# Kernel tuning notes

Hardware: AMD Instinct MI355X
Metric: run time of the kernel (lower is better)

Reference implementation:

```python
import jax, jax.numpy as jnp
import numpy as np

B, L, N, D, H, DFF, LAYERS, PRED = 16, 96, 512, 512, 8, 2048, 2, 96
NMARK = 4
WINDOWS = (4, 8, 12, 24)
EPS_REVIN = 1e-5


def layernorm(x, g, b, eps=1e-5):
    m = x.mean(-1, keepdims=True)
    v = ((x - m) ** 2).mean(-1, keepdims=True)
    return (x - m) * jax.lax.rsqrt(v + eps) * g + b


def moving_avg(x, w):
    # replicate-pad left by w-1, then window-mean of size w (stride 1) -> same length
    p = jnp.pad(x, ((0, 0), (w - 1, 0), (0, 0)), mode='edge')
    c = jnp.cumsum(p, axis=1)
    c = jnp.concatenate([jnp.zeros_like(c[:, :1]), c], axis=1)
    return (c[:, w:] - c[:, :-w]) / w


def trend_guidance(x, w1, b1, w2, b2):
    # x: [B, L, N]
    trend_stack = jnp.stack([moving_avg(x, w) for w in WINDOWS], axis=-1)  # [B,L,N,W]
    mean_f = x.mean(axis=1)
    std_f = jnp.sqrt(x.var(axis=1) + 1e-6)
    stats = jnp.stack([mean_f, std_f], axis=-1)  # [B,N,2]
    h = jax.nn.relu(stats @ w1 + b1)
    weights = jax.nn.softmax(h @ w2 + b2, axis=-1)  # [B,N,W]
    trend = (trend_stack * weights[:, None]).sum(-1)  # [B,L,N]
    tf = trend.transpose(0, 2, 1)  # [B,N,L]
    nt = tf / jnp.maximum(jnp.linalg.norm(tf, axis=-1, keepdims=True), 1e-12)
    return nt @ nt.transpose(0, 2, 1)  # [B,N,N]


def enc_layer(x, guide_full, wq, bq, wk, bk, wv, bv, wo, bo, w1, b1, w2, b2, l1g, l1b, l2g, l2b):
    Bq, T, Dm = x.shape
    E = Dm // H
    q = (x @ wq + bq).reshape(Bq, T, H, E)
    k = (x @ wk + bk).reshape(Bq, T, H, E)
    v = (x @ wv + bv).reshape(Bq, T, H, E)
    scores = jnp.einsum('blhe,bshe->bhls', q, k) / jnp.sqrt(jnp.asarray(E, x.dtype))
    attn = jax.nn.softmax(scores, axis=-1)
    attn = attn * guide_full[:, None]                      # sigmoid guidance gate
    attn = attn / (attn.sum(-1, keepdims=True) + 1e-6)     # renormalize
    ctx = jnp.einsum('bhls,bshd->blhd', attn, v).reshape(Bq, T, Dm)
    x = x + (ctx @ wo + bo)
    x = layernorm(x, l1g, l1b)
    y = jax.nn.gelu(x @ w1 + b1, approximate=False)
    y = y @ w2 + b2
    return layernorm(x + y, l2g, l2b)


def setup_inputs():
    key = jax.random.key(0)
    ks = iter(jax.random.split(key, 64))
    def nrm(shape, s=0.02):
        return jax.random.normal(next(ks), shape, jnp.float32) * s
    return {
        'x_enc': jax.random.normal(next(ks), (B, L, N), jnp.float32),
        'x_mark_enc': jax.random.normal(next(ks), (B, L, NMARK), jnp.float32),
        'x_dec': jnp.zeros((1, 1, 1), jnp.float32),
        'x_mark_dec': jnp.zeros((1, 1, 1), jnp.float32),
        'gamma': jnp.ones((1, 1, N), jnp.float32),
        'beta': jnp.zeros((1, 1, N), jnp.float32),
        'tp_w1': nrm((2, 16), 0.5), 'tp_b1': jnp.zeros((16,), jnp.float32),
        'tp_w2': nrm((16, len(WINDOWS)), 0.5), 'tp_b2': jnp.zeros((len(WINDOWS),), jnp.float32),
        'emb_w': nrm((L, D)), 'emb_b': jnp.zeros((D,), jnp.float32),
        'wq': nrm((LAYERS, D, D)), 'bq': jnp.zeros((LAYERS, D), jnp.float32),
        'wk': nrm((LAYERS, D, D)), 'bk': jnp.zeros((LAYERS, D), jnp.float32),
        'wv': nrm((LAYERS, D, D)), 'bv': jnp.zeros((LAYERS, D), jnp.float32),
        'wo': nrm((LAYERS, D, D)), 'bo': jnp.zeros((LAYERS, D), jnp.float32),
        'w1': nrm((LAYERS, D, DFF)), 'b1': jnp.zeros((LAYERS, DFF), jnp.float32),
        'w2': nrm((LAYERS, DFF, D)), 'b2': jnp.zeros((LAYERS, D), jnp.float32),
        'ln1g': jnp.ones((LAYERS, D), jnp.float32), 'ln1b': jnp.zeros((LAYERS, D), jnp.float32),
        'ln2g': jnp.ones((LAYERS, D), jnp.float32), 'ln2b': jnp.zeros((LAYERS, D), jnp.float32),
        'normg': jnp.ones((D,), jnp.float32), 'normb': jnp.zeros((D,), jnp.float32),
        'proj_w': nrm((D, PRED)), 'proj_b': jnp.zeros((PRED,), jnp.float32),
    }


def reference(x_enc, x_mark_enc, x_dec, x_mark_dec, gamma, beta, tp_w1, tp_b1, tp_w2, tp_b2,
              emb_w, emb_b, wq, bq, wk, bk, wv, bv, wo, bo, w1, b1, w2, b2,
              ln1g, ln1b, ln2g, ln2b, normg, normb, proj_w, proj_b):
    Bq, Lq, Nq = x_enc.shape
    # RevIN
    mean = x_enc.mean(1, keepdims=True)
    std = jnp.sqrt(x_enc.var(1, keepdims=True) + EPS_REVIN)
    x_norm = (x_enc - mean) / std * gamma + beta
    # trend guidance [B,N,N]
    guidance = trend_guidance(x_norm, tp_w1, tp_b1, tp_w2, tp_b2)
    # inverted embedding: variates + time-mark features as tokens
    tok = jnp.concatenate([x_norm.transpose(0, 2, 1), x_mark_enc.transpose(0, 2, 1)], axis=1)  # [B,T,L]
    x = tok @ emb_w + emb_b  # [B,T,D]
    T = x.shape[1]
    guide_full = jnp.full((Bq, T, T), 0.5, x.dtype).at[:, :Nq, :Nq].set(jax.nn.sigmoid(guidance))
    for i in range(LAYERS):
        x = enc_layer(x, guide_full, wq[i], bq[i], wk[i], bk[i], wv[i], bv[i], wo[i], bo[i],
                      w1[i], b1[i], w2[i], b2[i], ln1g[i], ln1b[i], ln2g[i], ln2b[i])
    x = layernorm(x, normg, normb)
    dec = (x @ proj_w + proj_b).transpose(0, 2, 1)[:, :, :Nq]  # [B,pred_len,N]
    dec = (dec - beta) / (gamma + EPS_REVIN) * std + mean       # RevIN inverse
    return dec[:, -PRED:, :]
```

## Files before the change

### kernel.cpp

```cpp
#include <hip/hip_runtime.h>
#include <hip/hip_bf16.h>
#include <math.h>

#define B 16
#define L 96
#define N 512
#define D 512
#define H 8
#define E 64
#define DFF 2048
#define T 516
#define PRED 96
#define NMARK 4
#define VTS 576
#define NCHUNK 9

typedef __attribute__((ext_vector_type(8))) short bf16x8;
typedef __attribute__((ext_vector_type(4))) float f32x4;

#define WS_MEAN 0
#define WS_STD  32768
#define WS_GD   65536
#define WS_X    8454144
#define WS_XB   25362432
#define WS_WTS  33816576
#define WS_QB   46596096
#define WS_KB   55050240
#define WS_VT   63504384
#define VT_BYTES 9437184

#define WT_QKV  0u
#define WT_WO   1572864u
#define WT_W1   2097152u
#define WT_W2   4194304u
#define WT_EMB  6291456u
#define WT_PROJ 6340608u

__global__ void revin_stats_kernel(const float* __restrict__ x, float* __restrict__ mean,
                                   float* __restrict__ stdv) {
    int i = blockIdx.x * blockDim.x + threadIdx.x;
    if (i >= B * N) return;
    int b = i >> 9;
    int n = i & (N - 1);
    const float* p = x + (size_t)b * L * N + n;
    float s = 0.f, ss = 0.f;
    for (int l = 0; l < L; ++l) {
        float v = p[(size_t)l * N];
        s += v; ss += v * v;
    }
    float m = s / (float)L;
    float var = ss / (float)L - m * m;
    mean[i] = m;
    stdv[i] = sqrtf(fmaxf(var, 0.f) + 1e-5f);
}

__global__ void norm_transpose_kernel(const float* __restrict__ x, const float* __restrict__ mean,
                                      const float* __restrict__ stdv, const float* __restrict__ gamma,
                                      const float* __restrict__ beta, float* __restrict__ xt,
                                      __hip_bfloat16* __restrict__ tokb) {
    int idx = blockIdx.x * blockDim.x + threadIdx.x;
    if (idx >= B * N * L) return;
    int l = idx % L;
    int n = (idx / L) % N;
    int b = idx / (L * N);
    float v = x[((size_t)b * L + l) * N + n];
    int bn = b * N + n;
    float o = (v - mean[bn]) / stdv[bn] * gamma[n] + beta[n];
    xt[idx] = o;
    tokb[((size_t)b * T + n) * L + l] = __float2bfloat16(o);
}

__global__ void build_mark_kernel(const float* __restrict__ xmark, __hip_bfloat16* __restrict__ tok) {
    int idx = blockIdx.x * blockDim.x + threadIdx.x;
    if (idx >= B * NMARK * L) return;
    int l = idx % L;
    int t = (idx / L) % NMARK;
    int b = idx / (L * NMARK);
    tok[((size_t)b * T + N + t) * L + l] =
        __float2bfloat16(xmark[((size_t)b * L + l) * NMARK + t]);
}

__global__ void trend_nt_kernel(const float* __restrict__ xt, const float* __restrict__ tp_w1,
                                const float* __restrict__ tp_b1, const float* __restrict__ tp_w2,
                                const float* __restrict__ tp_b2, __hip_bfloat16* __restrict__ ntb) {
    int bn = blockIdx.x;
    __shared__ float xr[96];
    __shared__ float P[97];
    __shared__ float wt[4];
    __shared__ float tr[96];
    __shared__ float nrm;
    int tid = threadIdx.x;
    if (tid < 96) xr[tid] = xt[(size_t)bn * 96 + tid];
    __syncthreads();
    if (tid == 0) {
        float s = 0.f, ss = 0.f;
        P[0] = 0.f;
        for (int l = 0; l < 96; ++l) { s += xr[l]; P[l + 1] = s; ss += xr[l] * xr[l]; }
        float m = s / 96.f;
        float var = ss / 96.f - m * m;
        float sd = sqrtf(fmaxf(var, 0.f) + 1e-6f);
        float h[16];
        for (int j = 0; j < 16; ++j) {
            float t = m * tp_w1[j] + sd * tp_w1[16 + j] + tp_b1[j];
            h[j] = fmaxf(t, 0.f);
        }
        float lg[4];
        for (int w = 0; w < 4; ++w) {
            float t = tp_b2[w];
            for (int j = 0; j < 16; ++j) t += h[j] * tp_w2[j * 4 + w];
            lg[w] = t;
        }
        float mx = fmaxf(fmaxf(lg[0], lg[1]), fmaxf(lg[2], lg[3]));
        float es = 0.f;
        for (int w = 0; w < 4; ++w) { lg[w] = expf(lg[w] - mx); es += lg[w]; }
        for (int w = 0; w < 4; ++w) wt[w] = lg[w] / es;
    }
    __syncthreads();
    const int WS[4] = {4, 8, 12, 24};
    if (tid < 96) {
        int l = tid;
        float t = 0.f;
        for (int wi = 0; wi < 4; ++wi) {
            int w = WS[wi];
            int lo = l - w + 1;
            float s;
            if (lo >= 0) s = P[l + 1] - P[lo];
            else         s = P[l + 1] - P[0] + (float)(-lo) * xr[0];
            t += (s / (float)w) * wt[wi];
        }
        tr[l] = t;
    }
    __syncthreads();
    if (tid == 0) {
        float s = 0.f;
        for (int l = 0; l < 96; ++l) s += tr[l] * tr[l];
        nrm = fmaxf(sqrtf(s), 1e-12f);
    }
    __syncthreads();
    if (tid < 96) ntb[(size_t)bn * 96 + tid] = __float2bfloat16(tr[tid] / nrm);
}

#define SWZM(row) (((row) >> 1) & 3)

__global__ __launch_bounds__(256, 2) void guide_mfma_kernel(
    const __hip_bfloat16* __restrict__ nt, __hip_bfloat16* __restrict__ gd) {
    __shared__ __align__(16) __hip_bfloat16 As[64 * 32];
    __shared__ __align__(16) __hip_bfloat16 Bs[64 * 32];
    int id = blockIdx.x;
    int b = id >> 6;
    int tile = id & 63;
    int bm = (tile >> 3) * 64;
    int bn = (tile & 7) * 64;
    const __hip_bfloat16* base = nt + (size_t)b * N * 96;
    int tid = threadIdx.x;
    int lane = tid & 63;
    int wave = tid >> 6;
    int col = lane & 15;
    int quad = lane >> 4;
    int wm = (wave & 1) * 32;
    int wn = (wave >> 1) * 32;
    f32x4 acc[2][2];
    #pragma unroll
    for (int i = 0; i < 2; ++i)
        #pragma unroll
        for (int j = 0; j < 2; ++j) acc[i][j] = (f32x4){0.f, 0.f, 0.f, 0.f};

    #pragma unroll
    for (int k0 = 0; k0 < 96; k0 += 32) {
        {
            int cbase = wave * 64;
            int c = cbase + lane;
            int row = c >> 2;
            int g = (c & 3) ^ SWZM(row);
            const __hip_bfloat16* ga = base + (size_t)(bm + row) * 96 + k0 + g * 8;
            __builtin_amdgcn_global_load_lds(
                (const __attribute__((address_space(1))) void*)ga,
                (__attribute__((address_space(3))) void*)(As + (size_t)cbase * 8), 16, 0, 0);
            const __hip_bfloat16* gb = base + (size_t)(bn + row) * 96 + k0 + g * 8;
            __builtin_amdgcn_global_load_lds(
                (const __attribute__((address_space(1))) void*)gb,
                (__attribute__((address_space(3))) void*)(Bs + (size_t)cbase * 8), 16, 0, 0);
        }
        __syncthreads();
        bf16x8 af[2], bfr[2];
        #pragma unroll
        for (int i = 0; i < 2; ++i) {
            int ra = wm + i * 16 + col;
            af[i] = *(const bf16x8*)(const void*)&As[(ra * 4 + (quad ^ SWZM(ra))) * 8];
        }
        #pragma unroll
        for (int j = 0; j < 2; ++j) {
            int rb = wn + j * 16 + col;
            bfr[j] = *(const bf16x8*)(const void*)&Bs[(rb * 4 + (quad ^ SWZM(rb))) * 8];
        }
        #pragma unroll
        for (int i = 0; i < 2; ++i)
            #pragma unroll
            for (int j = 0; j < 2; ++j)
                acc[i][j] = __builtin_amdgcn_mfma_f32_16x16x32_bf16(af[i], bfr[j], acc[i][j], 0, 0, 0);
        __syncthreads();
    }
    #pragma unroll
    for (int i = 0; i < 2; ++i) {
        int gmb = bm + wm + i * 16 + quad * 4;
        #pragma unroll
        for (int j = 0; j < 2; ++j) {
            int gn = bn + wn + j * 16 + col;
            #pragma unroll
            for (int r = 0; r < 4; ++r) {
                int gm = gmb + r;
                float sig = 1.f / (1.f + __expf(-acc[i][j][r]));
                gd[((size_t)b * N + gm) * N + gn] = __float2bfloat16(sig);
            }
        }
    }
}

__global__ void wconv_kernel(const float* __restrict__ wq, const float* __restrict__ wk,
                             const float* __restrict__ wv, const float* __restrict__ wo,
                             const float* __restrict__ w1, const float* __restrict__ w2,
                             const float* __restrict__ emb, const float* __restrict__ proj,
                             __hip_bfloat16* __restrict__ wts) {
    int bid = blockIdx.x;
    const float* src; __hip_bfloat16* dst; int K, Nn, tloc;
    if (bid < 2048) {
        int seg = bid >> 9;
        int t = bid & 511;
        int layer = t >> 8;
        tloc = t & 255;
        K = 512; Nn = 512;
        const float* bases[4] = {wq, wk, wv, wo};
        src = bases[seg] + (size_t)layer * 512 * 512;
        if (seg < 3)
            dst = wts + WT_QKV + (size_t)layer * 1536 * 512 + (size_t)seg * 512 * 512;
        else
            dst = wts + WT_WO + (size_t)layer * 512 * 512;
    } else if (bid < 4096) {
        int t = bid - 2048;
        int layer = t >> 10;
        tloc = t & 1023;
        K = 512; Nn = 2048;
        src = w1 + (size_t)layer * 512 * 2048;
        dst = wts + WT_W1 + (size_t)layer * 2048 * 512;
    } else if (bid < 6144) {
        int t = bid - 4096;
        int layer = t >> 10;
        tloc = t & 1023;
        K = 2048; Nn = 512;
        src = w2 + (size_t)layer * 2048 * 512;
        dst = wts + WT_W2 + (size_t)layer * 512 * 2048;
    } else if (bid < 6192) {
        tloc = bid - 6144;
        K = 96; Nn = 512;
        src = emb; dst = wts + WT_EMB;
    } else {
        tloc = bid - 6192;
        K = 512; Nn = 96;
        src = proj; dst = wts + WT_PROJ;
    }
    int ntile = Nn >> 5;
    int tk = tloc / ntile, tn = tloc % ntile;
    int k0 = tk * 32, n0 = tn * 32;
    __shared__ float ld[32][33];
    int tid = threadIdx.x;
    for (int i = tid; i < 1024; i += 256) {
        int r = i >> 5, c = i & 31;
        ld[r][c] = src[(size_t)(k0 + r) * Nn + n0 + c];
    }
    __syncthreads();
    for (int i = tid; i < 1024; i += 256) {
        int r = i >> 5, c = i & 31;
        dst[(size_t)(n0 + r) * K + k0 + c] = __float2bfloat16(ld[c][r]);
    }
}

__device__ __forceinline__ float gelu_tanh(float v) {
    float z = 0.7978845608028654f * (v + 0.044715f * v * v * v);
    float e = __expf(2.f * fabsf(z));
    float th = 1.f - 2.f / (e + 1.f);
    return 0.5f * v * (1.f + copysignf(th, z));
}

template<int TM, int TN>
__global__ __launch_bounds__(256, 2) void mfma_gemm_t(
    const __hip_bfloat16* __restrict__ A, const __hip_bfloat16* __restrict__ Wt,
    const float* __restrict__ bias, const __hip_bfloat16* __restrict__ resB,
    __hip_bfloat16* __restrict__ outB,
    int M, int Nn, int K, int act, int nbm, int nbn) {
    constexpr int WM = TM / 2, WN = TN / 2;
    constexpr int FI = WM / 16, FJ = WN / 16;
    __shared__ __align__(16) __hip_bfloat16 As[TM * 32];
    __shared__ __align__(16) __hip_bfloat16 Bs[TN * 32];
    int id = blockIdx.x;
    int xcd = id & 7, slot = id >> 3;
    int bmb = xcd + 8 * (slot / nbn);
    int bnb = slot % nbn;
    if (bmb >= nbm) return;
    int bm = bmb * TM;
    int bn = bnb * TN;
    int tid = threadIdx.x;
    int lane = tid & 63;
    int wave = tid >> 6;
    int col = lane & 15;
    int quad = lane >> 4;
    int wm = (wave & 1) * WM;
    int wn = (wave >> 1) * WN;
    f32x4 acc[FI][FJ];
    #pragma unroll
    for (int i = 0; i < FI; ++i)
        #pragma unroll
        for (int j = 0; j < FJ; ++j) acc[i][j] = (f32x4){0.f, 0.f, 0.f, 0.f};

    for (int k0 = 0; k0 < K; k0 += 32) {
        #pragma unroll
        for (int it = 0; it < TM / 64; ++it) {
            int cbase = it * 256 + wave * 64;
            int c = cbase + lane;
            int row = c >> 2;
            int g = (c & 3) ^ SWZM(row);
            int gm = bm + row; if (gm >= M) gm = M - 1;
            const __hip_bfloat16* ga = A + (size_t)gm * K + k0 + g * 8;
            __builtin_amdgcn_global_load_lds(
                (const __attribute__((address_space(1))) void*)ga,
                (__attribute__((address_space(3))) void*)(As + (size_t)cbase * 8), 16, 0, 0);
        }
        #pragma unroll
        for (int it = 0; it < TN / 64; ++it) {
            int cbase = it * 256 + wave * 64;
            int c = cbase + lane;
            int row = c >> 2;
            int g = (c & 3) ^ SWZM(row);
            int gn = bn + row; if (gn >= Nn) gn = Nn - 1;
            const __hip_bfloat16* gb = Wt + (size_t)gn * K + k0 + g * 8;
            __builtin_amdgcn_global_load_lds(
                (const __attribute__((address_space(1))) void*)gb,
                (__attribute__((address_space(3))) void*)(Bs + (size_t)cbase * 8), 16, 0, 0);
        }
        __syncthreads();
        bf16x8 af[FI], bfr[FJ];
        #pragma unroll
        for (int i = 0; i < FI; ++i) {
            int ra = wm + i * 16 + col;
            af[i] = *(const bf16x8*)(const void*)&As[(ra * 4 + (quad ^ SWZM(ra))) * 8];
        }
        #pragma unroll
        for (int j = 0; j < FJ; ++j) {
            int rb = wn + j * 16 + col;
            bfr[j] = *(const bf16x8*)(const void*)&Bs[(rb * 4 + (quad ^ SWZM(rb))) * 8];
        }
        #pragma unroll
        for (int i = 0; i < FI; ++i)
            #pragma unroll
            for (int j = 0; j < FJ; ++j)
                acc[i][j] = __builtin_amdgcn_mfma_f32_16x16x32_bf16(af[i], bfr[j], acc[i][j], 0, 0, 0);
        __syncthreads();
    }
    #pragma unroll
    for (int i = 0; i < FI; ++i) {
        int gmb = bm + wm + i * 16 + quad * 4;
        #pragma unroll
        for (int j = 0; j < FJ; ++j) {
            int gn = bn + wn + j * 16 + col;
            if (gn >= Nn) continue;
            float bs = bias[gn];
            #pragma unroll
            for (int r = 0; r < 4; ++r) {
                int gm = gmb + r;
                if (gm >= M) continue;
                float v = acc[i][j][r] + bs;
                if (act == 1) v = gelu_tanh(v);
                if (resB) v += __bfloat162float(resB[(size_t)gm * Nn + gn]);
                outB[(size_t)gm * Nn + gn] = __float2bfloat16(v);
            }
        }
    }
}

__global__ __launch_bounds__(256, 2) void qkv_gemm(
    const __hip_bfloat16* __restrict__ A, const __hip_bfloat16* __restrict__ Wt,
    const float* __restrict__ bq, const float* __restrict__ bk, const float* __restrict__ bv,
    __hip_bfloat16* __restrict__ qb, __hip_bfloat16* __restrict__ kb,
    __hip_bfloat16* __restrict__ vt, int nbm, int nbn) {
    const int M = B * T, K = D, Nn = 1536;
    __shared__ __align__(16) __hip_bfloat16 As[64 * 32];
    __shared__ __align__(16) __hip_bfloat16 Bs[64 * 32];
    int id = blockIdx.x;
    int xcd = id & 7, slot = id >> 3;
    int bmb = xcd + 8 * (slot / nbn);
    int bnb = slot % nbn;
    if (bmb >= nbm) return;
    int bm = bmb * 64;
    int bn = bnb * 64;
    int tid = threadIdx.x;
    int lane = tid & 63;
    int wave = tid >> 6;
    int col = lane & 15;
    int quad = lane >> 4;
    int wm = (wave & 1) * 32;
    int wn = (wave >> 1) * 32;
    f32x4 acc[2][2];
    #pragma unroll
    for (int i = 0; i < 2; ++i)
        #pragma unroll
        for (int j = 0; j < 2; ++j) acc[i][j] = (f32x4){0.f, 0.f, 0.f, 0.f};

    for (int k0 = 0; k0 < K; k0 += 32) {
        {
            int cbase = wave * 64;
            int c = cbase + lane;
            int row = c >> 2;
            int g = (c & 3) ^ SWZM(row);
            int gm = bm + row; if (gm >= M) gm = M - 1;
            const __hip_bfloat16* ga = A + (size_t)gm * K + k0 + g * 8;
            __builtin_amdgcn_global_load_lds(
                (const __attribute__((address_space(1))) void*)ga,
                (__attribute__((address_space(3))) void*)(As + (size_t)cbase * 8), 16, 0, 0);
            int gn = bn + row;
            const __hip_bfloat16* gb = Wt + (size_t)gn * K + k0 + g * 8;
            __builtin_amdgcn_global_load_lds(
                (const __attribute__((address_space(1))) void*)gb,
                (__attribute__((address_space(3))) void*)(Bs + (size_t)cbase * 8), 16, 0, 0);
        }
        __syncthreads();
        bf16x8 af[2], bfr[2];
        #pragma unroll
        for (int i = 0; i < 2; ++i) {
            int ra = wm + i * 16 + col;
            af[i] = *(const bf16x8*)(const void*)&As[(ra * 4 + (quad ^ SWZM(ra))) * 8];
        }
        #pragma unroll
        for (int j = 0; j < 2; ++j) {
            int rb = wn + j * 16 + col;
            bfr[j] = *(const bf16x8*)(const void*)&Bs[(rb * 4 + (quad ^ SWZM(rb))) * 8];
        }
        #pragma unroll
        for (int i = 0; i < 2; ++i)
            #pragma unroll
            for (int j = 0; j < 2; ++j)
                acc[i][j] = __builtin_amdgcn_mfma_f32_16x16x32_bf16(af[i], bfr[j], acc[i][j], 0, 0, 0);
        __syncthreads();
    }
    int sel = bn >> 9;
    const float* bias = sel == 0 ? bq : sel == 1 ? bk : bv;
    #pragma unroll
    for (int i = 0; i < 2; ++i) {
        int gmb = bm + wm + i * 16 + quad * 4;
        #pragma unroll
        for (int j = 0; j < 2; ++j) {
            int gn = bn + wn + j * 16 + col;
            int gl = gn & 511;
            float bs = bias[gl];
            #pragma unroll
            for (int r = 0; r < 4; ++r) {
                int gm = gmb + r;
                if (gm >= M) continue;
                float v = acc[i][j][r] + bs;
                if (sel == 0)      qb[(size_t)gm * 512 + gl] = __float2bfloat16(v);
                else if (sel == 1) kb[(size_t)gm * 512 + gl] = __float2bfloat16(v);
                else {
                    int bb = gm / T;
                    int tt = gm - bb * T;
                    vt[((size_t)bb * 512 + gl) * VTS + tt] = __float2bfloat16(v);
                }
            }
        }
    }
}

__global__ __launch_bounds__(256) void attn_flash_kernel(
    const __hip_bfloat16* __restrict__ qb, const __hip_bfloat16* __restrict__ kb,
    const __hip_bfloat16* __restrict__ vt, const __hip_bfloat16* __restrict__ gd,
    __hip_bfloat16* __restrict__ ctxb) {
    __shared__ __align__(16) __hip_bfloat16 Ks[64][72];
    __shared__ __align__(16) __hip_bfloat16 Vs[64][72];
    __shared__ __align__(16) __hip_bfloat16 Pw[4][16][72];
    __shared__ __align__(16) __hip_bfloat16 Gs[64][68];
    int bid = blockIdx.x;
    int sg = bid % 9;
    int h = (bid / 9) % H;
    int b = bid / (9 * H);
    int tid = threadIdx.x;
    int wave = tid >> 6, lane = tid & 63;
    int col = lane & 15, quad = lane >> 4;
    int q0b = sg * 64;
    int q0 = q0b + wave * 16;

    int qr = q0 + col; if (qr > T - 1) qr = T - 1;
    const __hip_bfloat16* qptr = qb + (size_t)(b * T + qr) * D + h * E + quad * 8;
    bf16x8 a0 = *(const bf16x8*)(const void*)qptr;
    bf16x8 a1 = *(const bf16x8*)(const void*)(qptr + 32);

    float S[4] = {0.f, 0.f, 0.f, 0.f};
    float G[4] = {0.f, 0.f, 0.f, 0.f};
    f32x4 o[4];
    #pragma unroll
    for (int j = 0; j < 4; ++j) o[j] = (f32x4){0.f, 0.f, 0.f, 0.f};

    const __hip_bfloat16* vbase = vt + (size_t)((b * H + h) * E) * VTS;

    for (int kc = 0; kc < NCHUNK; ++kc) {
        __syncthreads();
        #pragma unroll
        for (int i = 0; i < 2; ++i) {
            int idx = tid + i * 256;
            int r = idx >> 3, s = idx & 7;
            int kr = kc * 64 + r; int krc = kr > T - 1 ? T - 1 : kr;
            *(bf16x8*)(void*)&Ks[r][s * 8] =
                *(const bf16x8*)(const void*)(kb + (size_t)(b * T + krc) * D + h * E + s * 8);
            *(bf16x8*)(void*)&Vs[r][s * 8] =
                *(const bf16x8*)(const void*)(vbase + (size_t)r * VTS + kc * 64 + s * 8);
            bf16x8 gval;
            int grow = q0b + r;
            if (grow < N && kc < 8) {
                gval = *(const bf16x8*)(const void*)(gd + ((size_t)b * N + grow) * N + kc * 64 + s * 8);
            } else {
                gval = (bf16x8){0x3F00, 0x3F00, 0x3F00, 0x3F00, 0x3F00, 0x3F00, 0x3F00, 0x3F00};
            }
            *(bf16x8*)(void*)&Gs[r][s * 8] = gval;
        }
        __syncthreads();
        #pragma unroll
        for (int sub = 0; sub < 4; ++sub) {
            bf16x8 b0 = *(const bf16x8*)(const void*)&Ks[sub * 16 + col][quad * 8];
            bf16x8 b1 = *(const bf16x8*)(const void*)&Ks[sub * 16 + col][32 + quad * 8];
            f32x4 sc = (f32x4){0.f, 0.f, 0.f, 0.f};
            sc = __builtin_amdgcn_mfma_f32_16x16x32_bf16(a0, b0, sc, 0, 0, 0);
            sc = __builtin_amdgcn_mfma_f32_16x16x32_bf16(a1, b1, sc, 0, 0, 0);
            int key = kc * 64 + sub * 16 + col;
            #pragma unroll
            for (int r = 0; r < 4; ++r) {
                float v = sc[r] * 0.125f;
                if (key >= T) v = -1e30f;
                float p = __expf(v);
                S[r] += p;
                float g = __bfloat162float(Gs[wave * 16 + quad * 4 + r][sub * 16 + col]);
                float t = p * g;
                G[r] += t;
                Pw[wave][quad * 4 + r][sub * 16 + col] = __float2bfloat16(t);
            }
        }
        #pragma unroll
        for (int ks = 0; ks < 2; ++ks) {
            bf16x8 pa = *(const bf16x8*)(const void*)&Pw[wave][col][ks * 32 + quad * 8];
            #pragma unroll
            for (int j = 0; j < 4; ++j) {
                bf16x8 bv = *(const bf16x8*)(const void*)&Vs[j * 16 + col][ks * 32 + quad * 8];
                o[j] = __builtin_amdgcn_mfma_f32_16x16x32_bf16(pa, bv, o[j], 0, 0, 0);
            }
        }
    }
    #pragma unroll
    for (int r = 0; r < 4; ++r) {
        #pragma unroll
        for (int d = 1; d < 16; d <<= 1) {
            S[r] += __shfl_xor(S[r], d, 64);
            G[r] += __shfl_xor(G[r], d, 64);
        }
    }
    float inv[4];
    #pragma unroll
    for (int r = 0; r < 4; ++r) inv[r] = 1.f / (G[r] + 1e-6f * S[r]);
    #pragma unroll
    for (int j = 0; j < 4; ++j)
        #pragma unroll
        for (int r = 0; r < 4; ++r) {
            int row = q0 + quad * 4 + r;
            if (row < T)
                ctxb[(size_t)(b * T + row) * D + h * E + j * 16 + col] =
                    __float2bfloat16(o[j][r] * inv[r]);
        }
}

__global__ __launch_bounds__(256) void ln_kernel(__hip_bfloat16* __restrict__ xr,
                                                 const float* __restrict__ g,
                                                 const float* __restrict__ bb) {
    int row = blockIdx.x * 4 + (threadIdx.x >> 6);
    int lane = threadIdx.x & 63;
    __hip_bfloat16* base = xr + (size_t)row * D + lane * 8;
    __align__(16) __hip_bfloat16 u[8];
    *(bf16x8*)(void*)u = *(const bf16x8*)(const void*)base;
    float v[8];
    float s = 0.f, ss = 0.f;
    #pragma unroll
    for (int i = 0; i < 8; ++i) {
        v[i] = __bfloat162float(u[i]);
        s += v[i];
        ss += v[i] * v[i];
    }
    #pragma unroll
    for (int d = 1; d < 64; d <<= 1) {
        s += __shfl_xor(s, d, 64);
        ss += __shfl_xor(ss, d, 64);
    }
    float m = s * (1.f / (float)D);
    float var = ss * (1.f / (float)D) - m * m;
    float rstd = rsqrtf(fmaxf(var, 0.f) + 1e-5f);
    float4 g0 = *(const float4*)(g + lane * 8);
    float4 g1 = *(const float4*)(g + lane * 8 + 4);
    float4 b0 = *(const float4*)(bb + lane * 8);
    float4 b1 = *(const float4*)(bb + lane * 8 + 4);
    float gg[8] = {g0.x, g0.y, g0.z, g0.w, g1.x, g1.y, g1.z, g1.w};
    float bz[8] = {b0.x, b0.y, b0.z, b0.w, b1.x, b1.y, b1.z, b1.w};
    __align__(16) __hip_bfloat16 ot[8];
    #pragma unroll
    for (int i = 0; i < 8; ++i)
        ot[i] = __float2bfloat16((v[i] - m) * rstd * gg[i] + bz[i]);
    *(bf16x8*)(void*)base = *(const bf16x8*)(const void*)ot;
}

__global__ __launch_bounds__(256, 2) void proj_revin_gemm(
    const __hip_bfloat16* __restrict__ A, const __hip_bfloat16* __restrict__ Wt,
    const float* __restrict__ pb, const float* __restrict__ beta,
    const float* __restrict__ gamma, const float* __restrict__ mean,
    const float* __restrict__ stdv, float* __restrict__ out, int nbm, int nbn) {
    const int M = B * T, K = D, Nn = PRED;
    __shared__ __align__(16) __hip_bfloat16 As[64 * 32];
    __shared__ __align__(16) __hip_bfloat16 Bs[64 * 32];
    int id = blockIdx.x;
    int xcd = id & 7, slot = id >> 3;
    int bmb = xcd + 8 * (slot / nbn);
    int bnb = slot % nbn;
    if (bmb >= nbm) return;
    int bm = bmb * 64;
    int bn = bnb * 64;
    int tid = threadIdx.x;
    int lane = tid & 63;
    int wave = tid >> 6;
    int col = lane & 15;
    int quad = lane >> 4;
    int wm = (wave & 1) * 32;
    int wn = (wave >> 1) * 32;
    f32x4 acc[2][2];
    #pragma unroll
    for (int i = 0; i < 2; ++i)
        #pragma unroll
        for (int j = 0; j < 2; ++j) acc[i][j] = (f32x4){0.f, 0.f, 0.f, 0.f};

    for (int k0 = 0; k0 < K; k0 += 32) {
        {
            int cbase = wave * 64;
            int c = cbase + lane;
            int row = c >> 2;
            int g = (c & 3) ^ SWZM(row);
            int gm = bm + row; if (gm >= M) gm = M - 1;
            const __hip_bfloat16* ga = A + (size_t)gm * K + k0 + g * 8;
            __builtin_amdgcn_global_load_lds(
                (const __attribute__((address_space(1))) void*)ga,
                (__attribute__((address_space(3))) void*)(As + (size_t)cbase * 8), 16, 0, 0);
            int gn = bn + row; if (gn >= Nn) gn = Nn - 1;
            const __hip_bfloat16* gb = Wt + (size_t)gn * K + k0 + g * 8;
            __builtin_amdgcn_global_load_lds(
                (const __attribute__((address_space(1))) void*)gb,
                (__attribute__((address_space(3))) void*)(Bs + (size_t)cbase * 8), 16, 0, 0);
        }
        __syncthreads();
        bf16x8 af[2], bfr[2];
        #pragma unroll
        for (int i = 0; i < 2; ++i) {
            int ra = wm + i * 16 + col;
            af[i] = *(const bf16x8*)(const void*)&As[(ra * 4 + (quad ^ SWZM(ra))) * 8];
        }
        #pragma unroll
        for (int j = 0; j < 2; ++j) {
            int rb = wn + j * 16 + col;
            bfr[j] = *(const bf16x8*)(const void*)&Bs[(rb * 4 + (quad ^ SWZM(rb))) * 8];
        }
        #pragma unroll
        for (int i = 0; i < 2; ++i)
            #pragma unroll
            for (int j = 0; j < 2; ++j)
                acc[i][j] = __builtin_amdgcn_mfma_f32_16x16x32_bf16(af[i], bfr[j], acc[i][j], 0, 0, 0);
        __syncthreads();
    }
    #pragma unroll
    for (int i = 0; i < 2; ++i) {
        int gmb = bm + wm + i * 16 + quad * 4;
        int b = gmb / T;
        int n0 = gmb - b * T;
        #pragma unroll
        for (int j = 0; j < 2; ++j) {
            int gn = bn + wn + j * 16 + col;
            if (gn >= PRED) continue;
            float bs = pb[gn];
            #pragma unroll
            for (int r = 0; r < 4; ++r) {
                int gm = gmb + r;
                if (gm >= M) continue;
                int n = n0 + r;
                if (n >= N) continue;
                int bn_ = b * N + n;
                float v = acc[i][j][r] + bs;
                out[((size_t)b * PRED + gn) * N + n] =
                    (v - beta[n]) * (stdv[bn_] / (gamma[n] + 1e-5f)) + mean[bn_];
            }
        }
    }
}

static inline int swz_grid(int nbm, int nbn) { return 8 * ((nbm + 7) / 8) * nbn; }

extern "C" void kernel_launch(void* const* d_in, const int* in_sizes, int n_in,
                              void* d_out, int out_size, void* d_ws, size_t ws_size,
                              hipStream_t stream) {
    const float* x_enc  = (const float*)d_in[0];
    const float* x_mark = (const float*)d_in[1];
    const float* gamma  = (const float*)d_in[4];
    const float* beta   = (const float*)d_in[5];
    const float* tp_w1  = (const float*)d_in[6];
    const float* tp_b1  = (const float*)d_in[7];
    const float* tp_w2  = (const float*)d_in[8];
    const float* tp_b2  = (const float*)d_in[9];
    const float* emb_w  = (const float*)d_in[10];
    const float* emb_b  = (const float*)d_in[11];
    const float* wq = (const float*)d_in[12];
    const float* bq = (const float*)d_in[13];
    const float* wk = (const float*)d_in[14];
    const float* bk = (const float*)d_in[15];
    const float* wv = (const float*)d_in[16];
    const float* bv = (const float*)d_in[17];
    const float* wo = (const float*)d_in[18];
    const float* bo = (const float*)d_in[19];
    const float* w1 = (const float*)d_in[20];
    const float* b1 = (const float*)d_in[21];
    const float* w2 = (const float*)d_in[22];
    const float* b2 = (const float*)d_in[23];
    const float* ln1g = (const float*)d_in[24];
    const float* ln1b = (const float*)d_in[25];
    const float* ln2g = (const float*)d_in[26];
    const float* ln2b = (const float*)d_in[27];
    const float* normg = (const float*)d_in[28];
    const float* normb = (const float*)d_in[29];
    const float* proj_w = (const float*)d_in[30];
    const float* proj_b = (const float*)d_in[31];

    char* ws = (char*)d_ws;
    float* mean = (float*)(ws + WS_MEAN);
    float* stdv = (float*)(ws + WS_STD);
    __hip_bfloat16* gd  = (__hip_bfloat16*)(ws + WS_GD);
    __hip_bfloat16* R   = (__hip_bfloat16*)(ws + WS_X);
    __hip_bfloat16* ctxb = (__hip_bfloat16*)(ws + WS_XB);
    __hip_bfloat16* wts = (__hip_bfloat16*)(ws + WS_WTS);
    __hip_bfloat16* qbuf = (__hip_bfloat16*)(ws + WS_QB);
    __hip_bfloat16* kbuf = (__hip_bfloat16*)(ws + WS_KB);
    __hip_bfloat16* vt   = (__hip_bfloat16*)(ws + WS_VT);
    float* xt  = (float*)(ws + WS_KB);
    __hip_bfloat16* ntb = (__hip_bfloat16*)(ws + WS_VT);
    __hip_bfloat16* tokb = (__hip_bfloat16*)(ws + WS_QB);
    __hip_bfloat16* ffnb = (__hip_bfloat16*)(ws + WS_QB);

    revin_stats_kernel<<<(B * N + 255) / 256, 256, 0, stream>>>(x_enc, mean, stdv);
    norm_transpose_kernel<<<(B * N * L + 255) / 256, 256, 0, stream>>>(x_enc, mean, stdv, gamma, beta,
                                                                       xt, tokb);
    build_mark_kernel<<<(B * NMARK * L + 255) / 256, 256, 0, stream>>>(x_mark, tokb);
    trend_nt_kernel<<<B * N, 128, 0, stream>>>(xt, tp_w1, tp_b1, tp_w2, tp_b2, ntb);
    guide_mfma_kernel<<<B * 64, 256, 0, stream>>>(ntb, gd);
    hipMemsetAsync(vt, 0, VT_BYTES, stream);
    wconv_kernel<<<6240, 256, 0, stream>>>(wq, wk, wv, wo, w1, w2, emb_w, proj_w, wts);

    const int M = B * T;
    const int NBM64 = (M + 63) / 64;
    const int NBM128 = (M + 127) / 128;
    mfma_gemm_t<64, 64><<<swz_grid(NBM64, 8), 256, 0, stream>>>(
        tokb, wts + WT_EMB, emb_b, nullptr, R, M, D, L, 0, NBM64, 8);
    for (int i = 0; i < 2; ++i) {
        const __hip_bfloat16* qkvT = wts + WT_QKV + (size_t)i * 1536 * 512;
        const __hip_bfloat16* woT  = wts + WT_WO + (size_t)i * D * D;
        qkv_gemm<<<swz_grid(NBM64, 24), 256, 0, stream>>>(
            R, qkvT, bq + i * D, bk + i * D, bv + i * D, qbuf, kbuf, vt, NBM64, 24);
        attn_flash_kernel<<<B * H * 9, 256, 0, stream>>>(qbuf, kbuf, vt, gd, ctxb);
        mfma_gemm_t<64, 64><<<swz_grid(NBM64, 8), 256, 0, stream>>>(
            ctxb, woT, bo + i * D, R, R, M, D, D, 0, NBM64, 8);
        ln_kernel<<<M / 4, 256, 0, stream>>>(R, ln1g + i * D, ln1b + i * D);
        mfma_gemm_t<128, 128><<<swz_grid(NBM128, 16), 256, 0, stream>>>(
            R, wts + WT_W1 + (size_t)i * DFF * D, b1 + i * DFF, nullptr,
            ffnb, M, DFF, D, 1, NBM128, 16);
        mfma_gemm_t<64, 64><<<swz_grid(NBM64, 8), 256, 0, stream>>>(
            ffnb, wts + WT_W2 + (size_t)i * DFF * D, b2 + i * D, R, R,
            M, D, DFF, 0, NBM64, 8);
        ln_kernel<<<M / 4, 256, 0, stream>>>(R, ln2g + i * D, ln2b + i * D);
    }
    ln_kernel<<<M / 4, 256, 0, stream>>>(R, normg, normb);
    proj_revin_gemm<<<swz_grid(NBM64, 2), 256, 0, stream>>>(
        R, wts + WT_PROJ, proj_b, beta, gamma, mean, stdv, (float*)d_out, NBM64, 2);
}
```

Before: 630.9 us.

## Double-buffer LDS in GEMM kernels and use fast reciprocal in GELU and sigmoid

The generic MFMA GEMM and the QKV GEMM now use two LDS buffers. The next K-tile's global-to-LDS load is issued right after the barrier, so it can overlap the current tile's MFMAs, and one barrier per iteration is removed. The tanh-GELU is rewritten in the equivalent form x*sigmoid(2z) using the hardware reciprocal, and the sigmoid gate in the guidance kernel also uses rcp in place of a full divide. The costs are twice the LDS per block, which may reduce occupancy, and a small loss of accuracy from the approximate reciprocal. The overlap also depends on the compiler not inserting a full wait on the asynchronous LDS loads before the reads.

Result: no change. 636.5 us (+0.9%).

```diff
diff --git a/kernel.cpp b/kernel.cpp
--- a/kernel.cpp
+++ b/kernel.cpp
@@ -209,7 +209,7 @@
             #pragma unroll
             for (int r = 0; r < 4; ++r) {
                 int gm = gmb + r;
-                float sig = 1.f / (1.f + __expf(-acc[i][j][r]));
+                float sig = __builtin_amdgcn_rcpf(1.f + __expf(-acc[i][j][r]));
                 gd[((size_t)b * N + gm) * N + gn] = __float2bfloat16(sig);
             }
         }
@@ -275,10 +275,9 @@
 }
 
 __device__ __forceinline__ float gelu_tanh(float v) {
-    float z = 0.7978845608028654f * (v + 0.044715f * v * v * v);
-    float e = __expf(2.f * fabsf(z));
-    float th = 1.f - 2.f / (e + 1.f);
-    return 0.5f * v * (1.f + copysignf(th, z));
+    float y = 1.5957691216057308f * v * fmaf(0.044715f, v * v, 1.f);
+    float e = __expf(-y);
+    return v * __builtin_amdgcn_rcpf(1.f + e);
 }
 
 template<int TM, int TN>
@@ -289,8 +288,8 @@
     int M, int Nn, int K, int act, int nbm, int nbn) {
     constexpr int WM = TM / 2, WN = TN / 2;
     constexpr int FI = WM / 16, FJ = WN / 16;
-    __shared__ __align__(16) __hip_bfloat16 As[TM * 32];
-    __shared__ __align__(16) __hip_bfloat16 Bs[TN * 32];
+    __shared__ __align__(16) __hip_bfloat16 As[2][TM * 32];
+    __shared__ __align__(16) __hip_bfloat16 Bs[2][TN * 32];
     int id = blockIdx.x;
     int xcd = id & 7, slot = id >> 3;
     int bmb = xcd + 8 * (slot / nbn);
@@ -311,7 +310,8 @@
         #pragma unroll
         for (int j = 0; j < FJ; ++j) acc[i][j] = (f32x4){0.f, 0.f, 0.f, 0.f};
 
-    for (int k0 = 0; k0 < K; k0 += 32) {
+    auto stage = [&](int itk, int bufi) {
+        int k0 = itk << 5;
         #pragma unroll
         for (int it = 0; it < TM / 64; ++it) {
             int cbase = it * 256 + wave * 64;
@@ -322,7 +322,7 @@
             const __hip_bfloat16* ga = A + (size_t)gm * K + k0 + g * 8;
             __builtin_amdgcn_global_load_lds(
                 (const __attribute__((address_space(1))) void*)ga,
-                (__attribute__((address_space(3))) void*)(As + (size_t)cbase * 8), 16, 0, 0);
+                (__attribute__((address_space(3))) void*)(As[bufi] + (size_t)cbase * 8), 16, 0, 0);
         }
         #pragma unroll
         for (int it = 0; it < TN / 64; ++it) {
@@ -334,26 +334,33 @@
             const __hip_bfloat16* gb = Wt + (size_t)gn * K + k0 + g * 8;
             __builtin_amdgcn_global_load_lds(
                 (const __attribute__((address_space(1))) void*)gb,
-                (__attribute__((address_space(3))) void*)(Bs + (size_t)cbase * 8), 16, 0, 0);
-        }
+                (__attribute__((address_space(3))) void*)(Bs[bufi] + (size_t)cbase * 8), 16, 0, 0);
+        }
+    };
+
+    const int nIt = K >> 5;
+    stage(0, 0);
+    for (int itk = 0; itk < nIt; ++itk) {
         __syncthreads();
+        if (itk + 1 < nIt) stage(itk + 1, (itk + 1) & 1);
+        const __hip_bfloat16* Ac = As[itk & 1];
+        const __hip_bfloat16* Bc = Bs[itk & 1];
         bf16x8 af[FI], bfr[FJ];
         #pragma unroll
         for (int i = 0; i < FI; ++i) {
             int ra = wm + i * 16 + col;
-            af[i] = *(const bf16x8*)(const void*)&As[(ra * 4 + (quad ^ SWZM(ra))) * 8];
+            af[i] = *(const bf16x8*)(const void*)&Ac[(ra * 4 + (quad ^ SWZM(ra))) * 8];
         }
         #pragma unroll
         for (int j = 0; j < FJ; ++j) {
             int rb = wn + j * 16 + col;
-            bfr[j] = *(const bf16x8*)(const void*)&Bs[(rb * 4 + (quad ^ SWZM(rb))) * 8];
+            bfr[j] = *(const bf16x8*)(const void*)&Bc[(rb * 4 + (quad ^ SWZM(rb))) * 8];
         }
         #pragma unroll
         for (int i = 0; i < FI; ++i)
             #pragma unroll
             for (int j = 0; j < FJ; ++j)
                 acc[i][j] = __builtin_amdgcn_mfma_f32_16x16x32_bf16(af[i], bfr[j], acc[i][j], 0, 0, 0);
-        __syncthreads();
     }
     #pragma unroll
     for (int i = 0; i < FI; ++i) {
@@ -381,9 +388,9 @@
     const float* __restrict__ bq, const float* __restrict__ bk, const float* __restrict__ bv,
     __hip_bfloat16* __restrict__ qb, __hip_bfloat16* __restrict__ kb,
     __hip_bfloat16* __restrict__ vt, int nbm, int nbn) {
-    const int M = B * T, K = D, Nn = 1536;
-    __shared__ __align__(16) __hip_bfloat16 As[64 * 32];
-    __shared__ __align__(16) __hip_bfloat16 Bs[64 * 32];
+    const int M = B * T, K = D;
+    __shared__ __align__(16) __hip_bfloat16 As[2][64 * 32];
+    __shared__ __align__(16) __hip_bfloat16 Bs[2][64 * 32];
     int id = blockIdx.x;
     int xcd = id & 7, slot = id >> 3;
     int bmb = xcd + 8 * (slot / nbn);
@@ -404,41 +411,47 @@
         #pragma unroll
         for (int j = 0; j < 2; ++j) acc[i][j] = (f32x4){0.f, 0.f, 0.f, 0.f};
 
-    for (int k0 = 0; k0 < K; k0 += 32) {
-        {
-            int cbase = wave * 64;
-            int c = cbase + lane;
-            int row = c >> 2;
-            int g = (c & 3) ^ SWZM(row);
-            int gm = bm + row; if (gm >= M) gm = M - 1;
-            const __hip_bfloat16* ga = A + (size_t)gm * K + k0 + g * 8;
-            __builtin_amdgcn_global_load_lds(
-                (const __attribute__((address_space(1))) void*)ga,
-                (__attribute__((address_space(3))) void*)(As + (size_t)cbase * 8), 16, 0, 0);
-            int gn = bn + row;
-            const __hip_bfloat16* gb = Wt + (size_t)gn * K + k0 + g * 8;
-            __builtin_amdgcn_global_load_lds(
-                (const __attribute__((address_space(1))) void*)gb,
-                (__attribute__((address_space(3))) void*)(Bs + (size_t)cbase * 8), 16, 0, 0);
-        }
+    auto stage = [&](int itk, int bufi) {
+        int k0 = itk << 5;
+        int cbase = wave * 64;
+        int c = cbase + lane;
+        int row = c >> 2;
+        int g = (c & 3) ^ SWZM(row);
+        int gm = bm + row; if (gm >= M) gm = M - 1;
+        const __hip_bfloat16* ga = A + (size_t)gm * K + k0 + g * 8;
+        __builtin_amdgcn_global_load_lds(
+            (const __attribute__((address_space(1))) void*)ga,
+            (__attribute__((address_space(3))) void*)(As[bufi] + (size_t)cbase * 8), 16, 0, 0);
+        int gn = bn + row;
+        const __hip_bfloat16* gb = Wt + (size_t)gn * K + k0 + g * 8;
+        __builtin_amdgcn_global_load_lds(
+            (const __attribute__((address_space(1))) void*)gb,
+            (__attribute__((address_space(3))) void*)(Bs[bufi] + (size_t)cbase * 8), 16, 0, 0);
+    };
+
+    const int nIt = K >> 5;
+    stage(0, 0);
+    for (int itk = 0; itk < nIt; ++itk) {
         __syncthreads();
+        if (itk + 1 < nIt) stage(itk + 1, (itk + 1) & 1);
+        const __hip_bfloat16* Ac = As[itk & 1];
+        const __hip_bfloat16* Bc = Bs[itk & 1];
         bf16x8 af[2], bfr[2];
         #pragma unroll
         for (int i = 0; i < 2; ++i) {
             int ra = wm + i * 16 + col;
-            af[i] = *(const bf16x8*)(const void*)&As[(ra * 4 + (quad ^ SWZM(ra))) * 8];
+            af[i] = *(const bf16x8*)(const void*)&Ac[(ra * 4 + (quad ^ SWZM(ra))) * 8];
         }
         #pragma unroll
         for (int j = 0; j < 2; ++j) {
             int rb = wn + j * 16 + col;
-            bfr[j] = *(const bf16x8*)(const void*)&Bs[(rb * 4 + (quad ^ SWZM(rb))) * 8];
+            bfr[j] = *(const bf16x8*)(const void*)&Bc[(rb * 4 + (quad ^ SWZM(rb))) * 8];
         }
         #pragma unroll
         for (int i = 0; i < 2; ++i)
             #pragma unroll
             for (int j = 0; j < 2; ++j)
                 acc[i][j] = __builtin_amdgcn_mfma_f32_16x16x32_bf16(af[i], bfr[j], acc[i][j], 0, 0, 0);
-        __syncthreads();
     }
     int sel = bn >> 9;
     const float* bias = sel == 0 ? bq : sel == 1 ? bk : bv;
```
